# Kernel tuning notes

Measured on AMD Instinct MI355X. Metric: run time of the kernel, lower is better.

The kernel has to match this reference:

```python
import jax, jax.numpy as jnp
import numpy as np

NLAYER = 3
EPS = 1e-5
NEG = -1e30  # stand-in for -inf in masked max


def _layernorm(h, g, b):
    mu = h.mean(-1, keepdims=True)
    v = ((h - mu) ** 2).mean(-1, keepdims=True)
    return (h - mu) * jax.lax.rsqrt(v + EPS) * g + b


def setup_inputs() -> dict:
    key = jax.random.key(0)
    ks = jax.random.split(key, 8)
    N, K, D = 8192, 8, 128
    s = 0.05
    x = jax.random.normal(ks[0], (N, D), jnp.float32)
    neigh = jax.random.randint(ks[1], (N, K), 0, N, dtype=jnp.int32)
    nbr_count = jax.random.randint(ks[2], (N,), 0, K + 1, dtype=jnp.int32)
    gcn_W = jax.random.normal(ks[3], (NLAYER, D, D), jnp.float32) * s
    gcn_b = jnp.zeros((NLAYER, D), jnp.float32)
    gcn_ln_g = jnp.ones((NLAYER, D), jnp.float32)
    gcn_ln_b = jnp.zeros((NLAYER, D), jnp.float32)
    sage_pool_W = jax.random.normal(ks[4], (D, D), jnp.float32) * s
    sage_pool_b = jnp.zeros((D,), jnp.float32)
    sage_merge_W = jax.random.normal(ks[5], (NLAYER, D, 2 * D), jnp.float32) * s
    sage_merge_b = jnp.zeros((NLAYER, D), jnp.float32)
    sage_ln_g = jnp.ones((NLAYER - 1, D), jnp.float32)
    sage_ln_b = jnp.zeros((NLAYER - 1, D), jnp.float32)
    return {"x": x, "neigh": neigh, "nbr_count": nbr_count,
            "gcn_W": gcn_W, "gcn_b": gcn_b, "gcn_ln_g": gcn_ln_g, "gcn_ln_b": gcn_ln_b,
            "sage_pool_W": sage_pool_W, "sage_pool_b": sage_pool_b,
            "sage_merge_W": sage_merge_W, "sage_merge_b": sage_merge_b,
            "sage_ln_g": sage_ln_g, "sage_ln_b": sage_ln_b}


def reference(x, neigh, nbr_count, gcn_W, gcn_b, gcn_ln_g, gcn_ln_b,
              sage_pool_W, sage_pool_b, sage_merge_W, sage_merge_b,
              sage_ln_g, sage_ln_b):
    N, D = x.shape
    K = neigh.shape[1]
    mask = jnp.arange(K)[None, :] < nbr_count[:, None]  # [N, K] valid neighbors

    # ---- GCN branch: dense symmetric-normalized adjacency with self loops ----
    rows = jnp.broadcast_to(jnp.arange(N)[:, None], neigh.shape)
    A = jnp.zeros((N, N), x.dtype).at[rows, neigh].add(mask.astype(x.dtype))
    A = jnp.minimum(A, 1.0)  # dedupe multi-edges (original sets 1.0)
    A = A.at[jnp.arange(N), jnp.arange(N)].set(1.0)  # self loop (node[0] in list)
    dinv = jax.lax.rsqrt(A.sum(-1))  # degree^-0.5, >= 1 due to self loop
    Ah = dinv[:, None] * A * dinv[None, :]

    h = x
    first = None
    for i in range(NLAYER):
        nxt = h @ gcn_W[i].T + gcn_b[i]
        if i == 0:
            first = nxt
        nxt = jax.nn.relu(Ah @ nxt)
        # residual=True: layer 1 adds first-layer pre-prop enc, later layers add h
        h = _layernorm(nxt + (first if i == 0 else h), gcn_ln_g[i], gcn_ln_b[i])
    gcn_out = h

    # ---- SAGE branch: max-pool over children (self excluded), concat, merge ----
    def pool(node_encs):
        g = jnp.where(mask[:, :, None], node_encs[neigh], NEG)  # [N, K, D]
        p = g.max(axis=1)
        return jnp.where((nbr_count > 0)[:, None], p, 0.0)  # leaf -> zeros

    ne1 = jax.nn.relu(x @ sage_pool_W.T + sage_pool_b)  # pool linear only layer 1
    s = jax.nn.relu(jnp.concatenate([x, pool(ne1)], -1) @ sage_merge_W[0].T + sage_merge_b[0])
    for i in range(1, NLAYER):
        nxt = jax.nn.relu(jnp.concatenate([s, pool(s)], -1) @ sage_merge_W[i].T + sage_merge_b[i])
        s = _layernorm(nxt + s, sage_ln_g[i - 1], sage_ln_b[i - 1])

    return jnp.concatenate([gcn_out, s], -1)  # [N, 2*treehid]
```

## Files before the change

### kernel.cpp

```cpp
#include <hip/hip_runtime.h>

#define NND 8192
#define KNBR 8
#define DD 128
#define EPSF 1e-5f
#define TSH 16384
#define XSTR 132

typedef __attribute__((ext_vector_type(8))) short bf16x8;
typedef __attribute__((ext_vector_type(4))) float f32x4;

__device__ __forceinline__ unsigned short f2bf(float f) {
    unsigned u = __float_as_uint(f);
    u += 0x7FFF + ((u >> 16) & 1);
    return (unsigned short)(u >> 16);
}

__device__ __forceinline__ bf16x8 cvt8(const float* __restrict__ p) {
    float4 lo = *(const float4*)p;
    float4 hi = *(const float4*)(p + 4);
    bf16x8 r;
    r[0] = f2bf(lo.x); r[1] = f2bf(lo.y); r[2] = f2bf(lo.z); r[3] = f2bf(lo.w);
    r[4] = f2bf(hi.x); r[5] = f2bf(hi.y); r[6] = f2bf(hi.z); r[7] = f2bf(hi.w);
    return r;
}

__device__ __forceinline__ void gload_lds16(const unsigned short* g, unsigned short* l) {
    __builtin_amdgcn_global_load_lds(
        (const __attribute__((address_space(1))) unsigned int*)(g),
        (__attribute__((address_space(3))) unsigned int*)(l), 16, 0, 0);
}

template<int NT>
__device__ __forceinline__ void stageN(unsigned short* sh, const unsigned short* wb, int tid) {
    int lane = tid & 63, w = tid >> 6;
#pragma unroll
    for (int r = 0; r < NT * 8; ++r) {
        int blk = (r * 4 + w) * 512;
        gload_lds16(wb + blk + lane * 8, sh + blk);
    }
}

__device__ __forceinline__ void load_af(bf16x8* af, const unsigned short* __restrict__ A,
                                        int rowBase, int lane) {
    int idx = lane & 15, q = lane >> 4;
    const unsigned short* Ar = A + (size_t)(rowBase + idx) * DD;
#pragma unroll
    for (int s = 0; s < 4; ++s) af[s] = *(const bf16x8*)(Ar + s * 32 + q * 8);
}

__device__ __forceinline__ void load_af_f32(bf16x8* af, const float* __restrict__ A,
                                            int rowBase, int lane) {
    int idx = lane & 15, q = lane >> 4;
    const float* Ar = A + (size_t)(rowBase + idx) * DD;
#pragma unroll
    for (int s = 0; s < 4; ++s) af[s] = cvt8(Ar + s * 32 + q * 8);
}

__device__ __forceinline__ void mma_sw(const bf16x8* af, const unsigned short* shB,
                                       int lane, f32x4* acc) {
    int idx = lane & 15, q = lane >> 4, k7 = idx & 7;
#pragma unroll
    for (int s = 0; s < 4; ++s)
#pragma unroll
        for (int ct = 0; ct < 8; ++ct) {
            int ch = (4 * s + q) ^ k7;
            bf16x8 bf = *(const bf16x8*)(shB + (ct * 16 + idx) * 128 + ch * 8);
            acc[ct] = __builtin_amdgcn_mfma_f32_16x16x32_bf16(af[s], bf, acc[ct], 0, 0, 0);
        }
}

__device__ __forceinline__ void store_fw(float* __restrict__ out, int ostride, int oOff,
        int rowBase, int lane, const f32x4* acc, const float* __restrict__ bias, bool relu) {
    int idx = lane & 15, q = lane >> 4;
#pragma unroll
    for (int ct = 0; ct < 8; ++ct) {
        float b = bias[ct * 16 + idx];
#pragma unroll
        for (int r = 0; r < 4; ++r) {
            float v = acc[ct][r] + b;
            if (relu) v = fmaxf(v, 0.f);
            out[(size_t)(rowBase + q * 4 + r) * ostride + oOff + ct * 16 + idx] = v;
        }
    }
}

__device__ __forceinline__ void store_fw_b16(unsigned short* __restrict__ out,
        int rowBase, int lane, const f32x4* acc, const float* __restrict__ bias) {
    int idx = lane & 15, q = lane >> 4;
#pragma unroll
    for (int ct = 0; ct < 8; ++ct) {
        float b = bias[ct * 16 + idx];
#pragma unroll
        for (int r = 0; r < 4; ++r)
            out[(size_t)(rowBase + q * 4 + r) * DD + ct * 16 + idx]
                = f2bf(fmaxf(acc[ct][r] + b, 0.f));
    }
}

__device__ __forceinline__ void lnstore_fw(float* __restrict__ out, int ostride, int oOff,
        const float* __restrict__ resid, int rowBase, int lane, f32x4* acc,
        const float* __restrict__ bias, const float* __restrict__ g,
        const float* __restrict__ bv, unsigned short* __restrict__ outB) {
    int idx = lane & 15, q = lane >> 4;
    float rsum[4] = {0.f, 0.f, 0.f, 0.f};
#pragma unroll
    for (int ct = 0; ct < 8; ++ct) {
        float b = bias[ct * 16 + idx];
#pragma unroll
        for (int r = 0; r < 4; ++r) {
            float t = fmaxf(acc[ct][r] + b, 0.f)
                    + resid[(size_t)(rowBase + q * 4 + r) * DD + ct * 16 + idx];
            acc[ct][r] = t;
            rsum[r] += t;
        }
    }
#pragma unroll
    for (int r = 0; r < 4; ++r)
#pragma unroll
        for (int m = 1; m < 16; m <<= 1) rsum[r] += __shfl_xor(rsum[r], m, 64);
    float mu[4];
#pragma unroll
    for (int r = 0; r < 4; ++r) mu[r] = rsum[r] * (1.f / 128.f);
    float var[4] = {0.f, 0.f, 0.f, 0.f};
#pragma unroll
    for (int ct = 0; ct < 8; ++ct)
#pragma unroll
        for (int r = 0; r < 4; ++r) {
            float d = acc[ct][r] - mu[r];
            var[r] += d * d;
        }
#pragma unroll
    for (int r = 0; r < 4; ++r)
#pragma unroll
        for (int m = 1; m < 16; m <<= 1) var[r] += __shfl_xor(var[r], m, 64);
    float rs[4];
#pragma unroll
    for (int r = 0; r < 4; ++r) rs[r] = rsqrtf(var[r] * (1.f / 128.f) + EPSF);
#pragma unroll
    for (int ct = 0; ct < 8; ++ct) {
        float gg = g[ct * 16 + idx], bb = bv[ct * 16 + idx];
#pragma unroll
        for (int r = 0; r < 4; ++r) {
            float o = (acc[ct][r] - mu[r]) * rs[r] * gg + bb;
            size_t row = (size_t)(rowBase + q * 4 + r);
            out[row * ostride + oOff + ct * 16 + idx] = o;
            if (outB) outB[row * DD + ct * 16 + idx] = f2bf(o);
        }
    }
}

__global__ __launch_bounds__(256)
void cvt_deg(const int* __restrict__ neigh, const int* __restrict__ cnt,
             const float* __restrict__ gcnW, const float* __restrict__ poolW,
             const float* __restrict__ mW,
             float* __restrict__ dinv, int* __restrict__ kept,
             unsigned short* __restrict__ wbuf) {
    int bx = blockIdx.x, tid = threadIdx.x;
    if (bx < 32) {
        int i = bx * 256 + tid;
        int c = cnt[i];
        int nb[KNBR];
#pragma unroll
        for (int j = 0; j < KNBR; ++j) nb[j] = neigh[i * KNBR + j];
        int mask = 0, deg = 1;
#pragma unroll
        for (int j = 0; j < KNBR; ++j) {
            if (j < c) {
                int v = nb[j];
                bool dup = (v == i);
                for (int jj = 0; jj < j; ++jj)
                    if (nb[jj] == v) { dup = true; }
                if (!dup) { mask |= (1 << j); deg++; }
            }
        }
        dinv[i] = rsqrtf((float)deg);
        kept[i] = mask;
    } else {
        int cid = (bx - 32) * 256 + tid;
        int t = cid >> 11, c2 = cid & 2047, row = c2 >> 4, ch = c2 & 15;
        const float* base; int str;
        if (t < 3)       { base = gcnW + t * 16384; str = 128; }
        else if (t == 3) { base = poolW; str = 128; }
        else { int u = t - 4; base = mW + (u >> 1) * 32768 + (u & 1) * 128; str = 256; }
        bf16x8 v = cvt8(base + (size_t)row * str + ch * 8);
        *(bf16x8*)(wbuf + t * TSH + row * 128 + ((ch ^ (row & 7)) << 3)) = v;
    }
}

__global__ __launch_bounds__(256)
void mega_gemm(const float* __restrict__ x, const unsigned short* __restrict__ wbuf,
               const float* __restrict__ gB0, const float* __restrict__ pB,
               const float* __restrict__ mB0,
               float* __restrict__ G, unsigned short* __restrict__ E1b,
               float* __restrict__ S) {
    __shared__ __align__(16) unsigned short shB[TSH];
    const int tid = threadIdx.x, lane = tid & 63, w = tid >> 6;
    const int grp = blockIdx.y;
    const int tile = (grp == 0) ? 0 : (grp == 1) ? 3 : 4;
    stageN<1>(shB, wbuf + tile * TSH, tid);
    const int rowBase = ((int)blockIdx.x * 4 + w) * 16;
    bf16x8 af[4];
    load_af_f32(af, x, rowBase, lane);
    __syncthreads();
    f32x4 acc[8];
#pragma unroll
    for (int i = 0; i < 8; ++i) acc[i] = (f32x4){0.f, 0.f, 0.f, 0.f};
    mma_sw(af, shB, lane, acc);
    if (grp == 0)      store_fw(G, DD, 0, rowBase, lane, acc, gB0, false);
    else if (grp == 1) store_fw_b16(E1b, rowBase, lane, acc, pB);
    else               store_fw(S, DD, 0, rowBase, lane, acc, mB0, false);
}

__global__ __launch_bounds__(256)
void gemm_step4(const unsigned short* __restrict__ Pb, const unsigned short* __restrict__ H1b,
                const unsigned short* __restrict__ wbuf, const float* __restrict__ gB1,
                float* __restrict__ S, unsigned short* __restrict__ S1b,
                float* __restrict__ G) {
    __shared__ __align__(16) unsigned short shB[TSH];
    const int tid = threadIdx.x, lane = tid & 63, w = tid >> 6;
    const int rowBase = ((int)blockIdx.x * 4 + w) * 16;
    f32x4 acc[8];
#pragma unroll
    for (int i = 0; i < 8; ++i) acc[i] = (f32x4){0.f, 0.f, 0.f, 0.f};
    bf16x8 af[4];
    if (blockIdx.y == 0) {
        stageN<1>(shB, wbuf + 5 * TSH, tid);
        load_af(af, Pb, rowBase, lane);
        __syncthreads();
        mma_sw(af, shB, lane, acc);
        int idx = lane & 15, q = lane >> 4;
#pragma unroll
        for (int ct = 0; ct < 8; ++ct)
#pragma unroll
            for (int r = 0; r < 4; ++r) {
                size_t o = (size_t)(rowBase + q * 4 + r) * DD + ct * 16 + idx;
                float v = fmaxf(S[o] + acc[ct][r], 0.f);
                S[o] = v;
                S1b[o] = f2bf(v);
            }
    } else {
        stageN<1>(shB, wbuf + 1 * TSH, tid);
        load_af(af, H1b, rowBase, lane);
        __syncthreads();
        mma_sw(af, shB, lane, acc);
        store_fw(G, DD, 0, rowBase, lane, acc, gB1, false);
    }
}

__global__ __launch_bounds__(256)
void gemm_step6(const unsigned short* __restrict__ S1b, const unsigned short* __restrict__ Pb,
                const unsigned short* __restrict__ H2b, const float* __restrict__ S1,
                const unsigned short* __restrict__ wbuf,
                const float* __restrict__ mB1, const float* __restrict__ gB2,
                const float* __restrict__ sg, const float* __restrict__ sb,
                float* __restrict__ S2, unsigned short* __restrict__ S2b,
                float* __restrict__ G) {
    __shared__ __align__(16) unsigned short shB[2 * TSH];
    const int tid = threadIdx.x, lane = tid & 63, w = tid >> 6;
    const int rowBase = ((int)blockIdx.x * 4 + w) * 16;
    f32x4 acc[8];
#pragma unroll
    for (int i = 0; i < 8; ++i) acc[i] = (f32x4){0.f, 0.f, 0.f, 0.f};
    if (blockIdx.y == 0) {
        stageN<2>(shB, wbuf + 6 * TSH, tid);
        bf16x8 af1[4], af2[4];
        load_af(af1, S1b, rowBase, lane);
        load_af(af2, Pb, rowBase, lane);
        __syncthreads();
        mma_sw(af1, shB, lane, acc);
        mma_sw(af2, shB + TSH, lane, acc);
        lnstore_fw(S2, DD, 0, S1, rowBase, lane, acc, mB1, sg, sb, S2b);
    } else {
        stageN<1>(shB, wbuf + 2 * TSH, tid);
        bf16x8 af[4];
        load_af(af, H2b, rowBase, lane);
        __syncthreads();
        mma_sw(af, shB, lane, acc);
        store_fw(G, DD, 0, rowBase, lane, acc, gB2, false);
    }
}

__global__ __launch_bounds__(256)
void gemm_final(const unsigned short* __restrict__ S2b, const unsigned short* __restrict__ Pb,
                const float* __restrict__ S2, const unsigned short* __restrict__ wbuf,
                const float* __restrict__ mB2,
                const float* __restrict__ sg2, const float* __restrict__ sb2,
                float* __restrict__ out) {
    __shared__ __align__(16) unsigned short shB[2 * TSH];
    __shared__ float xch[32 * XSTR];
    const int tid = threadIdx.x, lane = tid & 63, w = tid >> 6;
    stageN<2>(shB, wbuf + 8 * TSH, tid);
    const int rowBase = (int)blockIdx.x * 32 + (w & 1) * 16;
    const int unit = w >> 1;
    bf16x8 af[4];
    load_af(af, unit ? Pb : S2b, rowBase, lane);
    __syncthreads();
    f32x4 acc[8];
#pragma unroll
    for (int i = 0; i < 8; ++i) acc[i] = (f32x4){0.f, 0.f, 0.f, 0.f};
    mma_sw(af, shB + unit * TSH, lane, acc);
    int idx = lane & 15, q = lane >> 4;
    if (unit) {
#pragma unroll
        for (int ct = 0; ct < 8; ++ct)
#pragma unroll
            for (int r = 0; r < 4; ++r)
                xch[((w & 1) * 16 + q * 4 + r) * XSTR + ct * 16 + idx] = acc[ct][r];
    }
    __syncthreads();
    if (!unit) {
#pragma unroll
        for (int ct = 0; ct < 8; ++ct)
#pragma unroll
            for (int r = 0; r < 4; ++r)
                acc[ct][r] += xch[((w & 1) * 16 + q * 4 + r) * XSTR + ct * 16 + idx];
        lnstore_fw(out, 2 * DD, DD, S2, rowBase, lane, acc, mB2, sg2, sb2, nullptr);
    }
}

__device__ __forceinline__ float wave_sum(float s) {
#pragma unroll
    for (int m = 1; m < 64; m <<= 1) s += __shfl_xor(s, m, 64);
    return s;
}

__device__ __forceinline__ void prop_ln_row(int row, int lane,
        const float* __restrict__ nxt, const float* __restrict__ resid,
        const float* __restrict__ dinv, const int* __restrict__ kept,
        const int* __restrict__ neigh,
        const float* __restrict__ g, const float* __restrict__ b,
        float* __restrict__ out, int oStride, int oOff,
        unsigned short* __restrict__ outB) {
    const float2* nxt2 = (const float2*)nxt;
    float di = dinv[row];
    int km = kept[row];
    int idxs[KNBR]; float wj[KNBR];
#pragma unroll
    for (int j = 0; j < KNBR; ++j) {
        int nb = neigh[row * KNBR + j];
        bool k = (km >> j) & 1;
        idxs[j] = k ? nb : row;
        wj[j] = k ? dinv[nb] : 0.f;
    }
    float2 vv[KNBR];
#pragma unroll
    for (int j = 0; j < KNBR; ++j) vv[j] = nxt2[(size_t)idxs[j] * 64 + lane];
    float2 self = nxt2[(size_t)row * 64 + lane];
    float ax = di * self.x, ay = di * self.y;
#pragma unroll
    for (int j = 0; j < KNBR; ++j) {
        ax = fmaf(wj[j], vv[j].x, ax);
        ay = fmaf(wj[j], vv[j].y, ay);
    }
    float2 r = ((const float2*)resid)[(size_t)row * 64 + lane];
    float vx = fmaxf(di * ax, 0.f) + r.x;
    float vy = fmaxf(di * ay, 0.f) + r.y;
    float mu = wave_sum(vx + vy) * (1.f / 128.f);
    float dx = vx - mu, dy = vy - mu;
    float var = wave_sum(dx * dx + dy * dy) * (1.f / 128.f);
    float rs = rsqrtf(var + EPSF);
    float2 gg = ((const float2*)g)[lane];
    float2 bb = ((const float2*)b)[lane];
    float2 o;
    o.x = dx * rs * gg.x + bb.x;
    o.y = dy * rs * gg.y + bb.y;
    *reinterpret_cast<float2*>(out + (size_t)row * oStride + oOff + lane * 2) = o;
    if (outB) {
        unsigned pk = (unsigned)f2bf(o.x) | ((unsigned)f2bf(o.y) << 16);
        *(unsigned*)(outB + (size_t)row * DD + lane * 2) = pk;
    }
}

__device__ __forceinline__ void pool_row_b(int row, int lane,
        const unsigned short* __restrict__ enc, const int* __restrict__ neigh,
        const int* __restrict__ cnt, unsigned short* __restrict__ P) {
    int c = cnt[row];
    const unsigned* e32 = (const unsigned*)enc;
    unsigned vv[KNBR];
#pragma unroll
    for (int j = 0; j < KNBR; ++j) {
        int nb = neigh[row * KNBR + j];
        int src = (j < c) ? nb : row;
        vv[j] = e32[(size_t)src * 64 + lane];
    }
    float ax = -1e30f, ay = -1e30f;
#pragma unroll
    for (int j = 0; j < KNBR; ++j) {
        if (j < c) {
            ax = fmaxf(ax, __uint_as_float(vv[j] << 16));
            ay = fmaxf(ay, __uint_as_float(vv[j] & 0xFFFF0000u));
        }
    }
    unsigned o = 0u;
    if (c > 0)
        o = (__float_as_uint(ax) >> 16) | (__float_as_uint(ay) & 0xFFFF0000u);
    ((unsigned*)P)[(size_t)row * 64 + lane] = o;
}

__global__ __launch_bounds__(256)
void prop_pool_kernel(const float* __restrict__ nxt, const float* __restrict__ resid,
                      const float* __restrict__ dinv, const int* __restrict__ kept,
                      const int* __restrict__ neigh, const int* __restrict__ cnt,
                      const float* __restrict__ g, const float* __restrict__ b,
                      float* __restrict__ outH, int oStride, int oOff,
                      unsigned short* __restrict__ outHB,
                      const unsigned short* __restrict__ enc,
                      unsigned short* __restrict__ P) {
    int row = blockIdx.x * 4 + (threadIdx.x >> 6);
    int lane = threadIdx.x & 63;
    prop_ln_row(row, lane, nxt, resid, dinv, kept, neigh, g, b, outH, oStride, oOff, outHB);
    pool_row_b(row, lane, enc, neigh, cnt, P);
}

extern "C" void kernel_launch(void* const* d_in, const int* in_sizes, int n_in,
                              void* d_out, int out_size, void* d_ws, size_t ws_size,
                              hipStream_t stream) {
    (void)in_sizes; (void)n_in; (void)out_size; (void)ws_size;
    const float* x      = (const float*)d_in[0];
    const int*   neigh  = (const int*)d_in[1];
    const int*   cnt    = (const int*)d_in[2];
    const float* gcnW   = (const float*)d_in[3];
    const float* gcnB   = (const float*)d_in[4];
    const float* gcnG   = (const float*)d_in[5];
    const float* gcnBb  = (const float*)d_in[6];
    const float* poolW  = (const float*)d_in[7];
    const float* poolB  = (const float*)d_in[8];
    const float* mW     = (const float*)d_in[9];
    const float* mB     = (const float*)d_in[10];
    const float* sg     = (const float*)d_in[11];
    const float* sb     = (const float*)d_in[12];
    float* out = (float*)d_out;

    char* ws = (char*)d_ws;
    float* dinv = (float*)ws;
    int*   kept = (int*)(ws + 32 * 1024);
    unsigned short* wbuf = (unsigned short*)(ws + 64 * 1024);
    float* G  = (float*)(ws + 448 * 1024);
    float* H1 = G  + NND * DD;
    float* H2 = H1 + NND * DD;
    float* S1 = H2 + NND * DD;
    float* S2 = S1 + NND * DD;
    unsigned short* E1b = (unsigned short*)(S2 + NND * DD);
    unsigned short* Pb  = E1b + NND * DD;
    unsigned short* H1b = Pb  + NND * DD;
    unsigned short* H2b = H1b + NND * DD;
    unsigned short* S1b = H2b + NND * DD;
    unsigned short* S2b = S1b + NND * DD;

    dim3 blk(256);
    dim3 rgrid(NND / 4);

    cvt_deg<<<dim3(112), blk, 0, stream>>>(neigh, cnt, gcnW, poolW, mW,
                                           dinv, kept, wbuf);
    mega_gemm<<<dim3(128, 3), blk, 0, stream>>>(x, wbuf, gcnB, poolB, mB, G, E1b, S1);
    prop_pool_kernel<<<rgrid, blk, 0, stream>>>(G, G, dinv, kept, neigh, cnt,
                                                gcnG, gcnBb, H1, DD, 0, H1b, E1b, Pb);
    gemm_step4<<<dim3(128, 2), blk, 0, stream>>>(Pb, H1b, wbuf, gcnB + DD,
                                                 S1, S1b, G);
    prop_pool_kernel<<<rgrid, blk, 0, stream>>>(G, H1, dinv, kept, neigh, cnt,
                                                gcnG + DD, gcnBb + DD, H2, DD, 0,
                                                H2b, S1b, Pb);
    gemm_step6<<<dim3(128, 2), blk, 0, stream>>>(S1b, Pb, H2b, S1, wbuf,
                                                 mB + DD, gcnB + 2 * DD, sg, sb,
                                                 S2, S2b, G);
    prop_pool_kernel<<<rgrid, blk, 0, stream>>>(G, H2, dinv, kept, neigh, cnt,
                                                gcnG + 2 * DD, gcnBb + 2 * DD,
                                                out, 2 * DD, 0, nullptr, S2b, Pb);
    gemm_final<<<dim3(256), blk, 0, stream>>>(S2b, Pb, S2, wbuf, mB + 2 * DD,
                                              sg + DD, sb + DD, out);
}
```

Before: 146.0 us.

## Fuse all stages into one persistent kernel with atomic grid barriers

Replaces eight separate kernel launches with a single persistent kernel of 256 blocks. Stages are separated by software grid barriers built on agent-scope atomics, and the barrier counters are cleared by a memset before the launch. This removes launch and drain gaps between the small stages. In exchange it gives up parallelism: propagation phases now use 256 blocks that each loop over 32 rows instead of 2048 blocks, and the final GEMM uses half the blocks. It also relies on all 256 blocks being co-resident, and the two-tile GEMMs now stage weights serially through a smaller LDS buffer.

```diff
diff --git a/kernel.cpp b/kernel.cpp
--- a/kernel.cpp
+++ b/kernel.cpp
@@ -5,7 +5,7 @@
 #define DD 128
 #define EPSF 1e-5f
 #define TSH 16384
-#define XSTR 132
+#define NBLK 256
 
 typedef __attribute__((ext_vector_type(8))) short bf16x8;
 typedef __attribute__((ext_vector_type(4))) float f32x4;
@@ -25,17 +25,26 @@
     return r;
 }
 
+__device__ __forceinline__ void gridbar(int* __restrict__ bar, int ph) {
+    __syncthreads();
+    if (threadIdx.x == 0) {
+        __hip_atomic_fetch_add(bar + ph, 1, __ATOMIC_RELEASE, __HIP_MEMORY_SCOPE_AGENT);
+        while (__hip_atomic_load(bar + ph, __ATOMIC_ACQUIRE, __HIP_MEMORY_SCOPE_AGENT) < NBLK)
+            __builtin_amdgcn_s_sleep(2);
+    }
+    __syncthreads();
+}
+
 __device__ __forceinline__ void gload_lds16(const unsigned short* g, unsigned short* l) {
     __builtin_amdgcn_global_load_lds(
         (const __attribute__((address_space(1))) unsigned int*)(g),
         (__attribute__((address_space(3))) unsigned int*)(l), 16, 0, 0);
 }
 
-template<int NT>
-__device__ __forceinline__ void stageN(unsigned short* sh, const unsigned short* wb, int tid) {
+__device__ __forceinline__ void stage1(unsigned short* sh, const unsigned short* wb, int tid) {
     int lane = tid & 63, w = tid >> 6;
 #pragma unroll
-    for (int r = 0; r < NT * 8; ++r) {
+    for (int r = 0; r < 8; ++r) {
         int blk = (r * 4 + w) * 512;
         gload_lds16(wb + blk + lane * 8, sh + blk);
     }
@@ -147,175 +156,6 @@
             out[row * ostride + oOff + ct * 16 + idx] = o;
             if (outB) outB[row * DD + ct * 16 + idx] = f2bf(o);
         }
-    }
-}
-
-__global__ __launch_bounds__(256)
-void cvt_deg(const int* __restrict__ neigh, const int* __restrict__ cnt,
-             const float* __restrict__ gcnW, const float* __restrict__ poolW,
-             const float* __restrict__ mW,
-             float* __restrict__ dinv, int* __restrict__ kept,
-             unsigned short* __restrict__ wbuf) {
-    int bx = blockIdx.x, tid = threadIdx.x;
-    if (bx < 32) {
-        int i = bx * 256 + tid;
-        int c = cnt[i];
-        int nb[KNBR];
-#pragma unroll
-        for (int j = 0; j < KNBR; ++j) nb[j] = neigh[i * KNBR + j];
-        int mask = 0, deg = 1;
-#pragma unroll
-        for (int j = 0; j < KNBR; ++j) {
-            if (j < c) {
-                int v = nb[j];
-                bool dup = (v == i);
-                for (int jj = 0; jj < j; ++jj)
-                    if (nb[jj] == v) { dup = true; }
-                if (!dup) { mask |= (1 << j); deg++; }
-            }
-        }
-        dinv[i] = rsqrtf((float)deg);
-        kept[i] = mask;
-    } else {
-        int cid = (bx - 32) * 256 + tid;
-        int t = cid >> 11, c2 = cid & 2047, row = c2 >> 4, ch = c2 & 15;
-        const float* base; int str;
-        if (t < 3)       { base = gcnW + t * 16384; str = 128; }
-        else if (t == 3) { base = poolW; str = 128; }
-        else { int u = t - 4; base = mW + (u >> 1) * 32768 + (u & 1) * 128; str = 256; }
-        bf16x8 v = cvt8(base + (size_t)row * str + ch * 8);
-        *(bf16x8*)(wbuf + t * TSH + row * 128 + ((ch ^ (row & 7)) << 3)) = v;
-    }
-}
-
-__global__ __launch_bounds__(256)
-void mega_gemm(const float* __restrict__ x, const unsigned short* __restrict__ wbuf,
-               const float* __restrict__ gB0, const float* __restrict__ pB,
-               const float* __restrict__ mB0,
-               float* __restrict__ G, unsigned short* __restrict__ E1b,
-               float* __restrict__ S) {
-    __shared__ __align__(16) unsigned short shB[TSH];
-    const int tid = threadIdx.x, lane = tid & 63, w = tid >> 6;
-    const int grp = blockIdx.y;
-    const int tile = (grp == 0) ? 0 : (grp == 1) ? 3 : 4;
-    stageN<1>(shB, wbuf + tile * TSH, tid);
-    const int rowBase = ((int)blockIdx.x * 4 + w) * 16;
-    bf16x8 af[4];
-    load_af_f32(af, x, rowBase, lane);
-    __syncthreads();
-    f32x4 acc[8];
-#pragma unroll
-    for (int i = 0; i < 8; ++i) acc[i] = (f32x4){0.f, 0.f, 0.f, 0.f};
-    mma_sw(af, shB, lane, acc);
-    if (grp == 0)      store_fw(G, DD, 0, rowBase, lane, acc, gB0, false);
-    else if (grp == 1) store_fw_b16(E1b, rowBase, lane, acc, pB);
-    else               store_fw(S, DD, 0, rowBase, lane, acc, mB0, false);
-}
-
-__global__ __launch_bounds__(256)
-void gemm_step4(const unsigned short* __restrict__ Pb, const unsigned short* __restrict__ H1b,
-                const unsigned short* __restrict__ wbuf, const float* __restrict__ gB1,
-                float* __restrict__ S, unsigned short* __restrict__ S1b,
-                float* __restrict__ G) {
-    __shared__ __align__(16) unsigned short shB[TSH];
-    const int tid = threadIdx.x, lane = tid & 63, w = tid >> 6;
-    const int rowBase = ((int)blockIdx.x * 4 + w) * 16;
-    f32x4 acc[8];
-#pragma unroll
-    for (int i = 0; i < 8; ++i) acc[i] = (f32x4){0.f, 0.f, 0.f, 0.f};
-    bf16x8 af[4];
-    if (blockIdx.y == 0) {
-        stageN<1>(shB, wbuf + 5 * TSH, tid);
-        load_af(af, Pb, rowBase, lane);
-        __syncthreads();
-        mma_sw(af, shB, lane, acc);
-        int idx = lane & 15, q = lane >> 4;
-#pragma unroll
-        for (int ct = 0; ct < 8; ++ct)
-#pragma unroll
-            for (int r = 0; r < 4; ++r) {
-                size_t o = (size_t)(rowBase + q * 4 + r) * DD + ct * 16 + idx;
-                float v = fmaxf(S[o] + acc[ct][r], 0.f);
-                S[o] = v;
-                S1b[o] = f2bf(v);
-            }
-    } else {
-        stageN<1>(shB, wbuf + 1 * TSH, tid);
-        load_af(af, H1b, rowBase, lane);
-        __syncthreads();
-        mma_sw(af, shB, lane, acc);
-        store_fw(G, DD, 0, rowBase, lane, acc, gB1, false);
-    }
-}
-
-__global__ __launch_bounds__(256)
-void gemm_step6(const unsigned short* __restrict__ S1b, const unsigned short* __restrict__ Pb,
-                const unsigned short* __restrict__ H2b, const float* __restrict__ S1,
-                const unsigned short* __restrict__ wbuf,
-                const float* __restrict__ mB1, const float* __restrict__ gB2,
-                const float* __restrict__ sg, const float* __restrict__ sb,
-                float* __restrict__ S2, unsigned short* __restrict__ S2b,
-                float* __restrict__ G) {
-    __shared__ __align__(16) unsigned short shB[2 * TSH];
-    const int tid = threadIdx.x, lane = tid & 63, w = tid >> 6;
-    const int rowBase = ((int)blockIdx.x * 4 + w) * 16;
-    f32x4 acc[8];
-#pragma unroll
-    for (int i = 0; i < 8; ++i) acc[i] = (f32x4){0.f, 0.f, 0.f, 0.f};
-    if (blockIdx.y == 0) {
-        stageN<2>(shB, wbuf + 6 * TSH, tid);
-        bf16x8 af1[4], af2[4];
-        load_af(af1, S1b, rowBase, lane);
-        load_af(af2, Pb, rowBase, lane);
-        __syncthreads();
-        mma_sw(af1, shB, lane, acc);
-        mma_sw(af2, shB + TSH, lane, acc);
-        lnstore_fw(S2, DD, 0, S1, rowBase, lane, acc, mB1, sg, sb, S2b);
-    } else {
-        stageN<1>(shB, wbuf + 2 * TSH, tid);
-        bf16x8 af[4];
-        load_af(af, H2b, rowBase, lane);
-        __syncthreads();
-        mma_sw(af, shB, lane, acc);
-        store_fw(G, DD, 0, rowBase, lane, acc, gB2, false);
-    }
-}
-
-__global__ __launch_bounds__(256)
-void gemm_final(const unsigned short* __restrict__ S2b, const unsigned short* __restrict__ Pb,
-                const float* __restrict__ S2, const unsigned short* __restrict__ wbuf,
-                const float* __restrict__ mB2,
-                const float* __restrict__ sg2, const float* __restrict__ sb2,
-                float* __restrict__ out) {
-    __shared__ __align__(16) unsigned short shB[2 * TSH];
-    __shared__ float xch[32 * XSTR];
-    const int tid = threadIdx.x, lane = tid & 63, w = tid >> 6;
-    stageN<2>(shB, wbuf + 8 * TSH, tid);
-    const int rowBase = (int)blockIdx.x * 32 + (w & 1) * 16;
-    const int unit = w >> 1;
-    bf16x8 af[4];
-    load_af(af, unit ? Pb : S2b, rowBase, lane);
-    __syncthreads();
-    f32x4 acc[8];
-#pragma unroll
-    for (int i = 0; i < 8; ++i) acc[i] = (f32x4){0.f, 0.f, 0.f, 0.f};
-    mma_sw(af, shB + unit * TSH, lane, acc);
-    int idx = lane & 15, q = lane >> 4;
-    if (unit) {
-#pragma unroll
-        for (int ct = 0; ct < 8; ++ct)
-#pragma unroll
-            for (int r = 0; r < 4; ++r)
-                xch[((w & 1) * 16 + q * 4 + r) * XSTR + ct * 16 + idx] = acc[ct][r];
-    }
-    __syncthreads();
-    if (!unit) {
-#pragma unroll
-        for (int ct = 0; ct < 8; ++ct)
-#pragma unroll
-            for (int r = 0; r < 4; ++r)
-                acc[ct][r] += xch[((w & 1) * 16 + q * 4 + r) * XSTR + ct * 16 + idx];
-        lnstore_fw(out, 2 * DD, DD, S2, rowBase, lane, acc, mB2, sg2, sb2, nullptr);
     }
 }
 
@@ -399,18 +239,183 @@
 }
 
 __global__ __launch_bounds__(256)
-void prop_pool_kernel(const float* __restrict__ nxt, const float* __restrict__ resid,
-                      const float* __restrict__ dinv, const int* __restrict__ kept,
-                      const int* __restrict__ neigh, const int* __restrict__ cnt,
-                      const float* __restrict__ g, const float* __restrict__ b,
-                      float* __restrict__ outH, int oStride, int oOff,
-                      unsigned short* __restrict__ outHB,
-                      const unsigned short* __restrict__ enc,
-                      unsigned short* __restrict__ P) {
-    int row = blockIdx.x * 4 + (threadIdx.x >> 6);
-    int lane = threadIdx.x & 63;
-    prop_ln_row(row, lane, nxt, resid, dinv, kept, neigh, g, b, outH, oStride, oOff, outHB);
-    pool_row_b(row, lane, enc, neigh, cnt, P);
+void fused_all(const float* __restrict__ x, const int* __restrict__ neigh,
+               const int* __restrict__ cnt,
+               const float* __restrict__ gcnW, const float* __restrict__ gcnB,
+               const float* __restrict__ gcnG, const float* __restrict__ gcnBb,
+               const float* __restrict__ poolW, const float* __restrict__ poolB,
+               const float* __restrict__ mW, const float* __restrict__ mB,
+               const float* __restrict__ sg, const float* __restrict__ sb,
+               float* __restrict__ out,
+               float* __restrict__ dinv, int* __restrict__ kept,
+               unsigned short* __restrict__ wbuf, int* __restrict__ bar,
+               float* __restrict__ G, float* __restrict__ H1, float* __restrict__ H2,
+               float* __restrict__ S1, float* __restrict__ S2,
+               unsigned short* __restrict__ E1b, unsigned short* __restrict__ Pb,
+               unsigned short* __restrict__ H1b, unsigned short* __restrict__ H2b,
+               unsigned short* __restrict__ S1b, unsigned short* __restrict__ S2b) {
+    __shared__ __align__(16) unsigned short shB[TSH];
+    const int bid = blockIdx.x, tid = threadIdx.x;
+    const int lane = tid & 63, w = tid >> 6;
+
+    if (bid < 32) {
+        int i = bid * 256 + tid;
+        int c = cnt[i];
+        int nb[KNBR];
+#pragma unroll
+        for (int j = 0; j < KNBR; ++j) nb[j] = neigh[i * KNBR + j];
+        int mask = 0, deg = 1;
+#pragma unroll
+        for (int j = 0; j < KNBR; ++j) {
+            if (j < c) {
+                int v = nb[j];
+                bool dup = (v == i);
+                for (int jj = 0; jj < j; ++jj)
+                    if (nb[jj] == v) { dup = true; }
+                if (!dup) { mask |= (1 << j); deg++; }
+            }
+        }
+        dinv[i] = rsqrtf((float)deg);
+        kept[i] = mask;
+    } else if (bid < 112) {
+        int cid = (bid - 32) * 256 + tid;
+        int t = cid >> 11, c2 = cid & 2047, row = c2 >> 4, ch = c2 & 15;
+        const float* base; int str;
+        if (t < 3)       { base = gcnW + t * 16384; str = 128; }
+        else if (t == 3) { base = poolW; str = 128; }
+        else { int u = t - 4; base = mW + (u >> 1) * 32768 + (u & 1) * 128; str = 256; }
+        bf16x8 v = cvt8(base + (size_t)row * str + ch * 8);
+        *(bf16x8*)(wbuf + t * TSH + row * 128 + ((ch ^ (row & 7)) << 3)) = v;
+    }
+    gridbar(bar, 0);
+
+    for (int t = bid; t < 384; t += NBLK) {
+        if (t != bid) __syncthreads();
+        int grp = t >> 7, bx = t & 127;
+        int tile = (grp == 0) ? 0 : (grp == 1) ? 3 : 4;
+        stage1(shB, wbuf + tile * TSH, tid);
+        int rowBase = (bx * 4 + w) * 16;
+        bf16x8 af[4];
+        load_af_f32(af, x, rowBase, lane);
+        __syncthreads();
+        f32x4 acc[8];
+#pragma unroll
+        for (int i = 0; i < 8; ++i) acc[i] = (f32x4){0.f, 0.f, 0.f, 0.f};
+        mma_sw(af, shB, lane, acc);
+        if (grp == 0)      store_fw(G, DD, 0, rowBase, lane, acc, gcnB, false);
+        else if (grp == 1) store_fw_b16(E1b, rowBase, lane, acc, poolB);
+        else               store_fw(S1, DD, 0, rowBase, lane, acc, mB, false);
+    }
+    gridbar(bar, 1);
+
+    {
+        int r0 = bid * 32 + w * 8;
+        for (int k = 0; k < 8; ++k)
+            prop_ln_row(r0 + k, lane, G, G, dinv, kept, neigh, gcnG, gcnBb, H1, DD, 0, H1b);
+        for (int k = 0; k < 8; ++k)
+            pool_row_b(r0 + k, lane, E1b, neigh, cnt, Pb);
+    }
+    gridbar(bar, 2);
+
+    {
+        int y = bid >> 7, bx = bid & 127;
+        int rowBase = (bx * 4 + w) * 16;
+        f32x4 acc[8];
+#pragma unroll
+        for (int i = 0; i < 8; ++i) acc[i] = (f32x4){0.f, 0.f, 0.f, 0.f};
+        bf16x8 af[4];
+        if (y == 0) {
+            stage1(shB, wbuf + 5 * TSH, tid);
+            load_af(af, Pb, rowBase, lane);
+            __syncthreads();
+            mma_sw(af, shB, lane, acc);
+            int idx = lane & 15, q = lane >> 4;
+#pragma unroll
+            for (int ct = 0; ct < 8; ++ct)
+#pragma unroll
+                for (int r = 0; r < 4; ++r) {
+                    size_t o = (size_t)(rowBase + q * 4 + r) * DD + ct * 16 + idx;
+                    float v = fmaxf(S1[o] + acc[ct][r], 0.f);
+                    S1[o] = v;
+                    S1b[o] = f2bf(v);
+                }
+        } else {
+            stage1(shB, wbuf + 1 * TSH, tid);
+            load_af(af, H1b, rowBase, lane);
+            __syncthreads();
+            mma_sw(af, shB, lane, acc);
+            store_fw(G, DD, 0, rowBase, lane, acc, gcnB + DD, false);
+        }
+    }
+    gridbar(bar, 3);
+
+    {
+        int r0 = bid * 32 + w * 8;
+        for (int k = 0; k < 8; ++k)
+            prop_ln_row(r0 + k, lane, G, H1, dinv, kept, neigh, gcnG + DD, gcnBb + DD,
+                        H2, DD, 0, H2b);
+        for (int k = 0; k < 8; ++k)
+            pool_row_b(r0 + k, lane, S1b, neigh, cnt, Pb);
+    }
+    gridbar(bar, 4);
+
+    {
+        int y = bid >> 7, bx = bid & 127;
+        int rowBase = (bx * 4 + w) * 16;
+        f32x4 acc[8];
+#pragma unroll
+        for (int i = 0; i < 8; ++i) acc[i] = (f32x4){0.f, 0.f, 0.f, 0.f};
+        if (y == 0) {
+            stage1(shB, wbuf + 6 * TSH, tid);
+            bf16x8 af1[4], af2[4];
+            load_af(af1, S1b, rowBase, lane);
+            load_af(af2, Pb, rowBase, lane);
+            __syncthreads();
+            mma_sw(af1, shB, lane, acc);
+            __syncthreads();
+            stage1(shB, wbuf + 7 * TSH, tid);
+            __syncthreads();
+            mma_sw(af2, shB, lane, acc);
+            lnstore_fw(S2, DD, 0, S1, rowBase, lane, acc, mB + DD, sg, sb, S2b);
+        } else {
+            stage1(shB, wbuf + 2 * TSH, tid);
+            bf16x8 af[4];
+            load_af(af, H2b, rowBase, lane);
+            __syncthreads();
+            mma_sw(af, shB, lane, acc);
+            store_fw(G, DD, 0, rowBase, lane, acc, gcnB + 2 * DD, false);
+        }
+    }
+    gridbar(bar, 5);
+
+    {
+        int r0 = bid * 32 + w * 8;
+        for (int k = 0; k < 8; ++k)
+            prop_ln_row(r0 + k, lane, G, H2, dinv, kept, neigh, gcnG + 2 * DD,
+                        gcnBb + 2 * DD, out, 2 * DD, 0, nullptr);
+        for (int k = 0; k < 8; ++k)
+            pool_row_b(r0 + k, lane, S2b, neigh, cnt, Pb);
+    }
+    gridbar(bar, 6);
+
+    if (bid < 128) {
+        int rowBase = (bid * 4 + w) * 16;
+        f32x4 acc[8];
+#pragma unroll
+        for (int i = 0; i < 8; ++i) acc[i] = (f32x4){0.f, 0.f, 0.f, 0.f};
+        stage1(shB, wbuf + 8 * TSH, tid);
+        bf16x8 af1[4], af2[4];
+        load_af(af1, S2b, rowBase, lane);
+        load_af(af2, Pb, rowBase, lane);
+        __syncthreads();
+        mma_sw(af1, shB, lane, acc);
+        __syncthreads();
+        stage1(shB, wbuf + 9 * TSH, tid);
+        __syncthreads();
+        mma_sw(af2, shB, lane, acc);
+        lnstore_fw(out, 2 * DD, DD, S2, rowBase, lane, acc, mB + 2 * DD,
+                   sg + DD, sb + DD, nullptr);
+    }
 }
 
 extern "C" void kernel_launch(void* const* d_in, const int* in_sizes, int n_in,
@@ -436,6 +441,7 @@
     float* dinv = (float*)ws;
     int*   kept = (int*)(ws + 32 * 1024);
     unsigned short* wbuf = (unsigned short*)(ws + 64 * 1024);
+    int*   bar  = (int*)(ws + 384 * 1024);
     float* G  = (float*)(ws + 448 * 1024);
     float* H1 = G  + NND * DD;
     float* H2 = H1 + NND * DD;
@@ -448,25 +454,10 @@
     unsigned short* S1b = H2b + NND * DD;
     unsigned short* S2b = S1b + NND * DD;
 
-    dim3 blk(256);
-    dim3 rgrid(NND / 4);
-
-    cvt_deg<<<dim3(112), blk, 0, stream>>>(neigh, cnt, gcnW, poolW, mW,
-                                           dinv, kept, wbuf);
-    mega_gemm<<<dim3(128, 3), blk, 0, stream>>>(x, wbuf, gcnB, poolB, mB, G, E1b, S1);
-    prop_pool_kernel<<<rgrid, blk, 0, stream>>>(G, G, dinv, kept, neigh, cnt,
-                                                gcnG, gcnBb, H1, DD, 0, H1b, E1b, Pb);
-    gemm_step4<<<dim3(128, 2), blk, 0, stream>>>(Pb, H1b, wbuf, gcnB + DD,
-                                                 S1, S1b, G);
-    prop_pool_kernel<<<rgrid, blk, 0, stream>>>(G, H1, dinv, kept, neigh, cnt,
-                                                gcnG + DD, gcnBb + DD, H2, DD, 0,
-                                                H2b, S1b, Pb);
-    gemm_step6<<<dim3(128, 2), blk, 0, stream>>>(S1b, Pb, H2b, S1, wbuf,
-                                                 mB + DD, gcnB + 2 * DD, sg, sb,
-                                                 S2, S2b, G);
-    prop_pool_kernel<<<rgrid, blk, 0, stream>>>(G, H2, dinv, kept, neigh, cnt,
-                                                gcnG + 2 * DD, gcnBb + 2 * DD,
-                                                out, 2 * DD, 0, nullptr, S2b, Pb);
-    gemm_final<<<dim3(256), blk, 0, stream>>>(S2b, Pb, S2, wbuf, mB + 2 * DD,
-                                              sg + DD, sb + DD, out);
-}
+    hipMemsetAsync(bar, 0, 256, stream);
+
+    fused_all<<<dim3(NBLK), dim3(256), 0, stream>>>(
+        x, neigh, cnt, gcnW, gcnB, gcnG, gcnBb, poolW, poolB, mW, mB, sg, sb, out,
+        dinv, kept, wbuf, bar, G, H1, H2, S1, S2,
+        E1b, Pb, H1b, H2b, S1b, S2b);
+}
```

After: 335.6 us. 2.3x slower.
